# Performance work log

Hardware: AMD Instinct MI355X
Metric: run time of the kernel (lower is better)

## Reference

```python
import jax, jax.numpy as jnp
import numpy as np

D_K = 1024
HEADS = 16
HK = 64
HV = 64


def setup_inputs() -> dict:
    key = jax.random.key(0)
    ks = jax.random.split(key, 12)
    B, S = 4, 2048
    sc_in = 1.0 / np.sqrt(D_K)
    sc_u = 1.0 / np.sqrt(HV * HEADS)
    return {
        "q": jax.random.normal(ks[0], (B, S, D_K), jnp.float32),
        "k": jax.random.normal(ks[1], (B, S, D_K), jnp.float32),
        "v": jax.random.normal(ks[2], (B, S, D_K), jnp.float32),
        "Wq": jax.random.normal(ks[3], (D_K, HK * HEADS), jnp.float32) * sc_in,
        "bq": jax.random.normal(ks[4], (HK * HEADS,), jnp.float32) * sc_in,
        "Wk": jax.random.normal(ks[5], (D_K, HK * HEADS), jnp.float32) * sc_in,
        "bk": jax.random.normal(ks[6], (HK * HEADS,), jnp.float32) * sc_in,
        "Wv": jax.random.normal(ks[7], (D_K, HV * HEADS), jnp.float32) * sc_in,
        "bv": jax.random.normal(ks[8], (HV * HEADS,), jnp.float32) * sc_in,
        "Wu": jax.random.normal(ks[9], (HV * HEADS, D_K), jnp.float32) * sc_u,
        "bu": jax.random.normal(ks[10], (D_K,), jnp.float32) * sc_u,
    }


def reference(q, k, v, Wq, bq, Wk, bk, Wv, bv, Wu, bu):
    B, S, _ = q.shape
    # QKV projections, split heads: (B, S, H, dh) -> (B, H, S, dh)
    qh = (q @ Wq + bq).reshape(B, S, HEADS, HK).transpose(0, 2, 1, 3)
    kh = (k @ Wk + bk).reshape(B, S, HEADS, HK).transpose(0, 2, 1, 3)
    vh = (v @ Wv + bv).reshape(B, S, HEADS, HV).transpose(0, 2, 1, 3)
    # Naive attention: scores scaled by sqrt(head_size) as in Sdpa
    scores = jnp.einsum("bhqd,bhkd->bhqk", qh, kh) / jnp.sqrt(
        jnp.asarray(HK, qh.dtype)
    )
    attn = jax.nn.softmax(scores, axis=-1)
    out = jnp.einsum("bhqk,bhkd->bhqd", attn, vh)  # (B, H, S, HV)
    # Merge heads: (B, S, H*HV), then output projection
    merged = out.transpose(0, 2, 1, 3).reshape(B, S, HEADS * HV)
    return merged @ Wu + bu
```

## Files before the change

### kernel.cpp

```cpp
#include <hip/hip_runtime.h>

typedef __bf16 bf16;
typedef __bf16 bf16x8 __attribute__((ext_vector_type(8)));
typedef __bf16 bf16x4 __attribute__((ext_vector_type(4)));
typedef float  f32x4  __attribute__((ext_vector_type(4)));

#define GLD_LDS16(gp, lp) __builtin_amdgcn_global_load_lds( \
    (const __attribute__((address_space(1))) unsigned int*)(const void*)(gp), \
    (__attribute__((address_space(3))) unsigned int*)(void*)(lp), 16, 0, 0)

constexpr int BB = 4, SSEQ = 2048, DK = 1024, NH = 16, DH = 64;
constexpr int M = BB * SSEQ;

constexpr size_t SZ_X = (size_t)M * DK * 2;
constexpr size_t SZ_W = (size_t)DK * DK * 2;
constexpr size_t OFF_QBF = 0;
constexpr size_t OFF_KBF = OFF_QBF + SZ_X;
constexpr size_t OFF_VBF = OFF_KBF + SZ_X;
constexpr size_t OFF_WQT = OFF_VBF + SZ_X;
constexpr size_t OFF_WKT = OFF_WQT + SZ_W;
constexpr size_t OFF_WVT = OFF_WKT + SZ_W;
constexpr size_t OFF_WUT = OFF_WVT + SZ_W;
constexpr size_t OFF_QH  = OFF_WUT + SZ_W;
constexpr size_t OFF_KH  = OFF_QH + SZ_X;
constexpr size_t OFF_VTH = OFF_KH + SZ_X;
constexpr size_t OFF_MRG = OFF_VTH + SZ_X;

__global__ void cvt_x(const float* __restrict__ q, const float* __restrict__ k,
                      const float* __restrict__ v,
                      bf16* __restrict__ qb, bf16* __restrict__ kb, bf16* __restrict__ vb) {
    const float* s = (blockIdx.z == 0) ? q : (blockIdx.z == 1) ? k : v;
    bf16*        d = (blockIdx.z == 0) ? qb : (blockIdx.z == 1) ? kb : vb;
    size_t i = (size_t)blockIdx.x * blockDim.x + threadIdx.x;
    float4 val = ((const float4*)s)[i];
    bf16x4 o = { (bf16)val.x, (bf16)val.y, (bf16)val.z, (bf16)val.w };
    ((bf16x4*)d)[i] = o;
}

__global__ void cvt_wT(const float* __restrict__ wq, const float* __restrict__ wk,
                       const float* __restrict__ wv, const float* __restrict__ wu,
                       bf16* __restrict__ wqt, bf16* __restrict__ wkt,
                       bf16* __restrict__ wvt, bf16* __restrict__ wut) {
    const float* w = (blockIdx.z == 0) ? wq : (blockIdx.z == 1) ? wk
                   : (blockIdx.z == 2) ? wv : wu;
    bf16* o        = (blockIdx.z == 0) ? wqt : (blockIdx.z == 1) ? wkt
                   : (blockIdx.z == 2) ? wvt : wut;
    __shared__ float t[64][65];
    int tx = threadIdx.x & 63, ty = threadIdx.x >> 6;
    int bx = blockIdx.x * 64, by = blockIdx.y * 64;
#pragma unroll
    for (int r = 0; r < 16; r++) {
        int row = ty * 16 + r;
        t[row][tx] = w[(size_t)(by + row) * DK + bx + tx];
    }
    __syncthreads();
#pragma unroll
    for (int r = 0; r < 16; r++) {
        int row2 = ty * 16 + r;
        o[(size_t)(bx + row2) * DK + by + tx] = (bf16)t[tx][row2];
    }
}

struct GArg {
    const bf16* A; const bf16* BT; const float* bias; void* out; int mode; float oscale;
};

__global__ __launch_bounds__(512, 2) void gemm_bt(GArg g0, GArg g1, GArg g2) {
    GArg g;
    if (blockIdx.z == 0) g = g0; else if (blockIdx.z == 1) g = g1; else g = g2;
    __shared__ __attribute__((aligned(16))) bf16 As[2][128 * 64];
    __shared__ __attribute__((aligned(16))) bf16 Bs[2][256 * 64];
    const int tid = threadIdx.x;
    const int lane = tid & 63, wv = tid >> 6;
    const int wm = (wv >> 2) * 64;
    const int wn = (wv & 3) * 64;
    const int cl = lane & 15, qd = lane >> 4;
    const int x = (int)blockIdx.x;
    const int rowbase = ((x & 7) * 8 + ((x >> 3) & 7)) * 128;
    const int colbase = (x >> 6) * 256;

    f32x4 acc[4][4];
#pragma unroll
    for (int i = 0; i < 4; i++)
#pragma unroll
        for (int j = 0; j < 4; j++) acc[i][j] = f32x4{0.f, 0.f, 0.f, 0.f};

    const bool swapped = (g.mode == 1);

    auto stage = [&](int t, int buf) {
#pragma unroll
        for (int c = 0; c < 2; c++) {
            int L = c * 512 + tid;
            int row = L >> 3, s16 = L & 7;
            int sc = s16 ^ (row & 7);
            GLD_LDS16(g.A + (size_t)(rowbase + row) * DK + t * 64 + sc * 8, &As[buf][L * 8]);
        }
#pragma unroll
        for (int c = 0; c < 4; c++) {
            int L = c * 512 + tid;
            int row = L >> 3, s16 = L & 7;
            int sc = s16 ^ (row & 7);
            GLD_LDS16(g.BT + (size_t)(colbase + row) * DK + t * 64 + sc * 8, &Bs[buf][L * 8]);
        }
    };

    stage(0, 0);
    stage(1, 1);

    auto ktile = [&](int t, int cur, bool doStage, bool last) __attribute__((always_inline)) {
        if (last) asm volatile("s_waitcnt vmcnt(0)" ::: "memory");
        else      asm volatile("s_waitcnt vmcnt(6)" ::: "memory");
        asm volatile("s_barrier" ::: "memory");
        bf16x8 a0[4], b0[4], a1[4], b1[4];
#pragma unroll
        for (int i = 0; i < 4; i++)
            a0[i] = *(const bf16x8*)&As[cur][(wm + i * 16 + cl) * 64 + ((qd ^ (cl & 7)) * 8)];
#pragma unroll
        for (int j = 0; j < 4; j++)
            b0[j] = *(const bf16x8*)&Bs[cur][(wn + j * 16 + cl) * 64 + ((qd ^ (cl & 7)) * 8)];
#pragma unroll
        for (int i = 0; i < 4; i++)
            a1[i] = *(const bf16x8*)&As[cur][(wm + i * 16 + cl) * 64 + (((4 + qd) ^ (cl & 7)) * 8)];
#pragma unroll
        for (int j = 0; j < 4; j++)
            b1[j] = *(const bf16x8*)&Bs[cur][(wn + j * 16 + cl) * 64 + (((4 + qd) ^ (cl & 7)) * 8)];
        __builtin_amdgcn_s_setprio(1);
        if (swapped) {
#pragma unroll
            for (int i = 0; i < 4; i++)
#pragma unroll
                for (int j = 0; j < 4; j++)
                    acc[i][j] = __builtin_amdgcn_mfma_f32_16x16x32_bf16(b0[j], a0[i], acc[i][j], 0, 0, 0);
        } else {
#pragma unroll
            for (int i = 0; i < 4; i++)
#pragma unroll
                for (int j = 0; j < 4; j++)
                    acc[i][j] = __builtin_amdgcn_mfma_f32_16x16x32_bf16(a0[i], b0[j], acc[i][j], 0, 0, 0);
        }
        __builtin_amdgcn_s_setprio(0);
        asm volatile("s_waitcnt lgkmcnt(0)" ::: "memory");
        asm volatile("s_barrier" ::: "memory");
        if (doStage) stage(t + 2, cur);
        __builtin_amdgcn_s_setprio(1);
        if (swapped) {
#pragma unroll
            for (int i = 0; i < 4; i++)
#pragma unroll
                for (int j = 0; j < 4; j++)
                    acc[i][j] = __builtin_amdgcn_mfma_f32_16x16x32_bf16(b1[j], a1[i], acc[i][j], 0, 0, 0);
        } else {
#pragma unroll
            for (int i = 0; i < 4; i++)
#pragma unroll
                for (int j = 0; j < 4; j++)
                    acc[i][j] = __builtin_amdgcn_mfma_f32_16x16x32_bf16(a1[i], b1[j], acc[i][j], 0, 0, 0);
        }
        __builtin_amdgcn_s_setprio(0);
    };

    for (int t = 0; t < 14; ++t) ktile(t, t & 1, true, false);
    ktile(14, 0, false, false);
    ktile(15, 1, false, true);

    if (g.mode == 2) {
        float* out = (float*)g.out;
#pragma unroll
        for (int i = 0; i < 4; i++)
#pragma unroll
            for (int j = 0; j < 4; j++)
#pragma unroll
                for (int r = 0; r < 4; r++) {
                    int row = rowbase + wm + i * 16 + qd * 4 + r;
                    int col = colbase + wn + j * 16 + cl;
                    out[(size_t)row * DK + col] = (acc[i][j][r] + g.bias[col]) * g.oscale;
                }
    } else if (g.mode == 0) {
        bf16* out = (bf16*)g.out;
#pragma unroll
        for (int i = 0; i < 4; i++)
#pragma unroll
            for (int j = 0; j < 4; j++)
#pragma unroll
                for (int r = 0; r < 4; r++) {
                    int row = rowbase + wm + i * 16 + qd * 4 + r;
                    int col = colbase + wn + j * 16 + cl;
                    float v = (acc[i][j][r] + g.bias[col]) * g.oscale;
                    out[(size_t)row * DK + col] = (bf16)v;
                }
    } else {
        bf16* out = (bf16*)g.out;
#pragma unroll
        for (int i = 0; i < 4; i++)
#pragma unroll
            for (int j = 0; j < 4; j++)
#pragma unroll
                for (int r = 0; r < 4; r++) {
                    int colg = colbase + wn + j * 16 + qd * 4 + r;
                    int rowg = rowbase + wm + i * 16 + cl;
                    int b_ = rowg >> 11, s_ = rowg & 2047;
                    float v = (acc[i][j][r] + g.bias[colg]) * g.oscale;
                    out[((size_t)(b_ * NH + (colg >> 6)) * DH + (colg & 63)) * SSEQ + s_] = (bf16)v;
                }
    }
}

__global__ __launch_bounds__(256, 4) void attn(const bf16* __restrict__ Qh,
                                               const bf16* __restrict__ Kh,
                                               const bf16* __restrict__ VTh,
                                               bf16* __restrict__ mrg) {
    __shared__ __attribute__((aligned(16))) bf16 Ks[2][64 * 64];
    __shared__ __attribute__((aligned(16))) bf16 VTs[2][64 * 64];
    const int tid = threadIdx.x;
    const int lane = tid & 63, w = tid >> 6;
    const int cl = lane & 15, qd = lane >> 4;
    const int F = blockIdx.x;
    const int xcd = F & 7, slot = F >> 3;
    const int bh = xcd * 8 + (slot & 7);
    const int qt = slot >> 3;
    const int b_ = bh >> 4, h_ = bh & 15;
    const int qbase = qt * 128;
    const bf16* Qb = Qh + ((size_t)b_ * SSEQ) * DK + h_ * DH;
    const bf16* Kb = Kh + ((size_t)b_ * SSEQ) * DK + h_ * DH;
    const bf16* Vb = VTh + (size_t)bh * DH * SSEQ;

    bf16x8 qf[2][2];
#pragma unroll
    for (int mi = 0; mi < 2; mi++) {
        int q = qbase + w * 32 + mi * 16 + cl;
        qf[mi][0] = *(const bf16x8*)&Qb[(size_t)q * DK + qd * 8];
        qf[mi][1] = *(const bf16x8*)&Qb[(size_t)q * DK + 32 + qd * 8];
    }
    f32x4 O[2][4];
#pragma unroll
    for (int mi = 0; mi < 2; mi++)
#pragma unroll
        for (int jv = 0; jv < 4; jv++) O[mi][jv] = f32x4{0.f, 0.f, 0.f, 0.f};
    float ps[2] = {0.f, 0.f};

    auto stage = [&](int kt, int buf) {
#pragma unroll
        for (int c = 0; c < 2; c++) {
            int L = c * 256 + tid;
            int row = L >> 3, lc = (L & 7) ^ (row & 7);
            int prow = ((row >> 5) << 5) | (((row >> 2) & 3) << 3)
                     | (((row >> 4) & 1) << 2) | (row & 3);
            GLD_LDS16(Kb + (size_t)(kt * 64 + prow) * DK + lc * 8, &Ks[buf][L * 8]);
        }
#pragma unroll
        for (int c = 0; c < 2; c++) {
            int L = c * 256 + tid;
            int row = L >> 3, lc = (L & 7) ^ (row & 7);
            GLD_LDS16(Vb + (size_t)row * SSEQ + kt * 64 + lc * 8, &VTs[buf][L * 8]);
        }
    };
    stage(0, 0);

    for (int kt = 0; kt < 32; kt++) {
        const int buf = kt & 1;
        __syncthreads();
        if (kt + 1 < 32) stage(kt + 1, buf ^ 1);

        bf16x8 pf8[2][2];
#pragma unroll
        for (int jt = 0; jt < 4; jt++) {
            bf16x8 kf0 = *(const bf16x8*)&Ks[buf][(jt * 16 + cl) * 64 + ((qd ^ (cl & 7)) * 8)];
            bf16x8 kf1 = *(const bf16x8*)&Ks[buf][(jt * 16 + cl) * 64 + (((4 + qd) ^ (cl & 7)) * 8)];
#pragma unroll
            for (int mi = 0; mi < 2; mi++) {
                f32x4 S = __builtin_amdgcn_mfma_f32_16x16x32_bf16(kf0, qf[mi][0],
                                                                  f32x4{0.f, 0.f, 0.f, 0.f}, 0, 0, 0);
                S = __builtin_amdgcn_mfma_f32_16x16x32_bf16(kf1, qf[mi][1], S, 0, 0, 0);
                float s = 0.f;
#pragma unroll
                for (int r = 0; r < 4; r++) {
                    float p = __builtin_amdgcn_exp2f(S[r]);
                    s += p;
                    pf8[mi][jt >> 1][(jt & 1) * 4 + r] = (bf16)p;
                }
                ps[mi] += s;
            }
        }

#pragma unroll
        for (int g = 0; g < 2; g++) {
#pragma unroll
            for (int jv = 0; jv < 4; jv++) {
                bf16x8 vf = *(const bf16x8*)&VTs[buf][(jv * 16 + cl) * 64 +
                                (((g * 4 + qd) ^ (cl & 7)) * 8)];
#pragma unroll
                for (int mi = 0; mi < 2; mi++)
                    O[mi][jv] = __builtin_amdgcn_mfma_f32_16x16x32_bf16(vf, pf8[mi][g], O[mi][jv], 0, 0, 0);
            }
        }
    }

#pragma unroll
    for (int mi = 0; mi < 2; mi++) {
        float t = ps[mi];
        t += __shfl_xor(t, 16);
        t += __shfl_xor(t, 32);
        float inv = 1.0f / t;
        int q = qbase + w * 32 + mi * 16 + cl;
        size_t ro = ((size_t)(b_ * SSEQ + q)) * DK + h_ * DH;
#pragma unroll
        for (int jv = 0; jv < 4; jv++) {
            bf16x4 o4;
#pragma unroll
            for (int r = 0; r < 4; r++) o4[r] = (bf16)(O[mi][jv][r] * inv);
            *(bf16x4*)&mrg[ro + jv * 16 + qd * 4] = o4;
        }
    }
}

extern "C" void kernel_launch(void* const* d_in, const int* in_sizes, int n_in,
                              void* d_out, int out_size, void* d_ws, size_t ws_size,
                              hipStream_t stream) {
    const float* q  = (const float*)d_in[0];
    const float* k  = (const float*)d_in[1];
    const float* v  = (const float*)d_in[2];
    const float* Wq = (const float*)d_in[3];
    const float* bq = (const float*)d_in[4];
    const float* Wk = (const float*)d_in[5];
    const float* bk = (const float*)d_in[6];
    const float* Wv = (const float*)d_in[7];
    const float* bv = (const float*)d_in[8];
    const float* Wu = (const float*)d_in[9];
    const float* bu = (const float*)d_in[10];
    char* ws = (char*)d_ws;
    bf16* qbf = (bf16*)(ws + OFF_QBF);
    bf16* kbf = (bf16*)(ws + OFF_KBF);
    bf16* vbf = (bf16*)(ws + OFF_VBF);
    bf16* wqt = (bf16*)(ws + OFF_WQT);
    bf16* wkt = (bf16*)(ws + OFF_WKT);
    bf16* wvt = (bf16*)(ws + OFF_WVT);
    bf16* wut = (bf16*)(ws + OFF_WUT);
    bf16* qh  = (bf16*)(ws + OFF_QH);
    bf16* kh  = (bf16*)(ws + OFF_KH);
    bf16* vth = (bf16*)(ws + OFF_VTH);
    bf16* mrg = (bf16*)(ws + OFF_MRG);

    cvt_x<<<dim3(8192, 1, 3), 256, 0, stream>>>(q, k, v, qbf, kbf, vbf);
    cvt_wT<<<dim3(16, 16, 4), 256, 0, stream>>>(Wq, Wk, Wv, Wu, wqt, wkt, wvt, wut);

    GArg gq{qbf, wqt, bq, (void*)qh, 0, 0.18033688011112043f};
    GArg gk{kbf, wkt, bk, (void*)kh, 0, 1.0f};
    GArg gv{vbf, wvt, bv, (void*)vth, 1, 1.0f};
    gemm_bt<<<dim3(256, 1, 3), 512, 0, stream>>>(gq, gk, gv);

    attn<<<dim3(1024), 256, 0, stream>>>(qh, kh, vth, mrg);

    GArg go{mrg, wut, bu, d_out, 2, 1.0f};
    gemm_bt<<<dim3(256, 1, 1), 512, 0, stream>>>(go, go, go);
}
```

Measured before the change: 323.7 us.

## Fuse all stages into one persistent cooperative megakernel with grid syncs

Replaces the five separate launches (input convert, weight transpose, QKV GEMM, attention, output GEMM) with one cooperative persistent kernel whose stages are separated by grid.sync(). The GEMM tile shrinks from 128x256 to 128x128 to fit a shared 64KB LDS arena, and each 512-thread block runs two attention work items side by side. Priority hints are added around the attention MFMAs. The aim is to remove launch overhead and inter-kernel gaps, at the cost of grid-wide barriers, smaller GEMM tiles with less reuse, and a grid capped by occupancy.

```diff
diff --git a/kernel.cpp b/kernel.cpp
--- a/kernel.cpp
+++ b/kernel.cpp
@@ -1,4 +1,6 @@
 #include <hip/hip_runtime.h>
+#include <hip/hip_cooperative_groups.h>
+namespace cg = cooperative_groups;
 
 typedef __bf16 bf16;
 typedef __bf16 bf16x8 __attribute__((ext_vector_type(8)));
@@ -26,64 +28,33 @@
 constexpr size_t OFF_VTH = OFF_KH + SZ_X;
 constexpr size_t OFF_MRG = OFF_VTH + SZ_X;
 
-__global__ void cvt_x(const float* __restrict__ q, const float* __restrict__ k,
-                      const float* __restrict__ v,
-                      bf16* __restrict__ qb, bf16* __restrict__ kb, bf16* __restrict__ vb) {
-    const float* s = (blockIdx.z == 0) ? q : (blockIdx.z == 1) ? k : v;
-    bf16*        d = (blockIdx.z == 0) ? qb : (blockIdx.z == 1) ? kb : vb;
-    size_t i = (size_t)blockIdx.x * blockDim.x + threadIdx.x;
-    float4 val = ((const float4*)s)[i];
-    bf16x4 o = { (bf16)val.x, (bf16)val.y, (bf16)val.z, (bf16)val.w };
-    ((bf16x4*)d)[i] = o;
-}
-
-__global__ void cvt_wT(const float* __restrict__ wq, const float* __restrict__ wk,
-                       const float* __restrict__ wv, const float* __restrict__ wu,
-                       bf16* __restrict__ wqt, bf16* __restrict__ wkt,
-                       bf16* __restrict__ wvt, bf16* __restrict__ wut) {
-    const float* w = (blockIdx.z == 0) ? wq : (blockIdx.z == 1) ? wk
-                   : (blockIdx.z == 2) ? wv : wu;
-    bf16* o        = (blockIdx.z == 0) ? wqt : (blockIdx.z == 1) ? wkt
-                   : (blockIdx.z == 2) ? wvt : wut;
-    __shared__ float t[64][65];
-    int tx = threadIdx.x & 63, ty = threadIdx.x >> 6;
-    int bx = blockIdx.x * 64, by = blockIdx.y * 64;
-#pragma unroll
-    for (int r = 0; r < 16; r++) {
-        int row = ty * 16 + r;
-        t[row][tx] = w[(size_t)(by + row) * DK + bx + tx];
-    }
-    __syncthreads();
-#pragma unroll
-    for (int r = 0; r < 16; r++) {
-        int row2 = ty * 16 + r;
-        o[(size_t)(bx + row2) * DK + by + tx] = (bf16)t[tx][row2];
-    }
-}
 
 struct GArg {
     const bf16* A; const bf16* BT; const float* bias; void* out; int mode; float oscale;
 };
 
-__global__ __launch_bounds__(512, 2) void gemm_bt(GArg g0, GArg g1, GArg g2) {
-    GArg g;
-    if (blockIdx.z == 0) g = g0; else if (blockIdx.z == 1) g = g1; else g = g2;
-    __shared__ __attribute__((aligned(16))) bf16 As[2][128 * 64];
-    __shared__ __attribute__((aligned(16))) bf16 Bs[2][256 * 64];
-    const int tid = threadIdx.x;
+struct MegaArg {
+    const float *q, *k, *v, *wq, *wk, *wv, *wu;
+    const float *bq, *bk, *bv, *bu;
+    bf16 *qbf, *kbf, *vbf, *wqt, *wkt, *wvt, *wut, *qh, *kh, *vth, *mrg;
+    float* out;
+};
+
+__device__ __forceinline__ void gemm_tile(const GArg& g, int x, int tid, char* arena) {
+    bf16 (*As)[128 * 64] = (bf16(*)[128 * 64])arena;
+    bf16 (*Bs)[128 * 64] = (bf16(*)[128 * 64])(arena + 32768);
     const int lane = tid & 63, wv = tid >> 6;
     const int wm = (wv >> 2) * 64;
-    const int wn = (wv & 3) * 64;
+    const int wn = (wv & 3) * 32;
     const int cl = lane & 15, qd = lane >> 4;
-    const int x = (int)blockIdx.x;
     const int rowbase = ((x & 7) * 8 + ((x >> 3) & 7)) * 128;
-    const int colbase = (x >> 6) * 256;
-
-    f32x4 acc[4][4];
+    const int colbase = (x >> 6) * 128;
+
+    f32x4 acc[4][2];
 #pragma unroll
     for (int i = 0; i < 4; i++)
 #pragma unroll
-        for (int j = 0; j < 4; j++) acc[i][j] = f32x4{0.f, 0.f, 0.f, 0.f};
+        for (int j = 0; j < 2; j++) acc[i][j] = f32x4{0.f, 0.f, 0.f, 0.f};
 
     const bool swapped = (g.mode == 1);
 
@@ -96,7 +67,7 @@
             GLD_LDS16(g.A + (size_t)(rowbase + row) * DK + t * 64 + sc * 8, &As[buf][L * 8]);
         }
 #pragma unroll
-        for (int c = 0; c < 4; c++) {
+        for (int c = 0; c < 2; c++) {
             int L = c * 512 + tid;
             int row = L >> 3, s16 = L & 7;
             int sc = s16 ^ (row & 7);
@@ -109,33 +80,33 @@
 
     auto ktile = [&](int t, int cur, bool doStage, bool last) __attribute__((always_inline)) {
         if (last) asm volatile("s_waitcnt vmcnt(0)" ::: "memory");
-        else      asm volatile("s_waitcnt vmcnt(6)" ::: "memory");
+        else      asm volatile("s_waitcnt vmcnt(4)" ::: "memory");
         asm volatile("s_barrier" ::: "memory");
-        bf16x8 a0[4], b0[4], a1[4], b1[4];
+        bf16x8 a0[4], b0[2], a1[4], b1[2];
 #pragma unroll
         for (int i = 0; i < 4; i++)
             a0[i] = *(const bf16x8*)&As[cur][(wm + i * 16 + cl) * 64 + ((qd ^ (cl & 7)) * 8)];
 #pragma unroll
-        for (int j = 0; j < 4; j++)
+        for (int j = 0; j < 2; j++)
             b0[j] = *(const bf16x8*)&Bs[cur][(wn + j * 16 + cl) * 64 + ((qd ^ (cl & 7)) * 8)];
 #pragma unroll
         for (int i = 0; i < 4; i++)
             a1[i] = *(const bf16x8*)&As[cur][(wm + i * 16 + cl) * 64 + (((4 + qd) ^ (cl & 7)) * 8)];
 #pragma unroll
-        for (int j = 0; j < 4; j++)
+        for (int j = 0; j < 2; j++)
             b1[j] = *(const bf16x8*)&Bs[cur][(wn + j * 16 + cl) * 64 + (((4 + qd) ^ (cl & 7)) * 8)];
         __builtin_amdgcn_s_setprio(1);
         if (swapped) {
 #pragma unroll
             for (int i = 0; i < 4; i++)
 #pragma unroll
-                for (int j = 0; j < 4; j++)
+                for (int j = 0; j < 2; j++)
                     acc[i][j] = __builtin_amdgcn_mfma_f32_16x16x32_bf16(b0[j], a0[i], acc[i][j], 0, 0, 0);
         } else {
 #pragma unroll
             for (int i = 0; i < 4; i++)
 #pragma unroll
-                for (int j = 0; j < 4; j++)
+                for (int j = 0; j < 2; j++)
                     acc[i][j] = __builtin_amdgcn_mfma_f32_16x16x32_bf16(a0[i], b0[j], acc[i][j], 0, 0, 0);
         }
         __builtin_amdgcn_s_setprio(0);
@@ -147,13 +118,13 @@
 #pragma unroll
             for (int i = 0; i < 4; i++)
 #pragma unroll
-                for (int j = 0; j < 4; j++)
+                for (int j = 0; j < 2; j++)
                     acc[i][j] = __builtin_amdgcn_mfma_f32_16x16x32_bf16(b1[j], a1[i], acc[i][j], 0, 0, 0);
         } else {
 #pragma unroll
             for (int i = 0; i < 4; i++)
 #pragma unroll
-                for (int j = 0; j < 4; j++)
+                for (int j = 0; j < 2; j++)
                     acc[i][j] = __builtin_amdgcn_mfma_f32_16x16x32_bf16(a1[i], b1[j], acc[i][j], 0, 0, 0);
         }
         __builtin_amdgcn_s_setprio(0);
@@ -168,7 +139,7 @@
 #pragma unroll
         for (int i = 0; i < 4; i++)
 #pragma unroll
-            for (int j = 0; j < 4; j++)
+            for (int j = 0; j < 2; j++)
 #pragma unroll
                 for (int r = 0; r < 4; r++) {
                     int row = rowbase + wm + i * 16 + qd * 4 + r;
@@ -180,7 +151,7 @@
 #pragma unroll
         for (int i = 0; i < 4; i++)
 #pragma unroll
-            for (int j = 0; j < 4; j++)
+            for (int j = 0; j < 2; j++)
 #pragma unroll
                 for (int r = 0; r < 4; r++) {
                     int row = rowbase + wm + i * 16 + qd * 4 + r;
@@ -193,7 +164,7 @@
 #pragma unroll
         for (int i = 0; i < 4; i++)
 #pragma unroll
-            for (int j = 0; j < 4; j++)
+            for (int j = 0; j < 2; j++)
 #pragma unroll
                 for (int r = 0; r < 4; r++) {
                     int colg = colbase + wn + j * 16 + qd * 4 + r;
@@ -205,24 +176,19 @@
     }
 }
 
-__global__ __launch_bounds__(256, 4) void attn(const bf16* __restrict__ Qh,
-                                               const bf16* __restrict__ Kh,
-                                               const bf16* __restrict__ VTh,
-                                               bf16* __restrict__ mrg) {
-    __shared__ __attribute__((aligned(16))) bf16 Ks[2][64 * 64];
-    __shared__ __attribute__((aligned(16))) bf16 VTs[2][64 * 64];
-    const int tid = threadIdx.x;
-    const int lane = tid & 63, w = tid >> 6;
+__device__ __forceinline__ void attn_logical(int W, int ltid, char* slice, const MegaArg& A) {
+    bf16 (*Ks)[64 * 64]  = (bf16(*)[64 * 64])slice;
+    bf16 (*VTs)[64 * 64] = (bf16(*)[64 * 64])(slice + 16384);
+    const int lane = ltid & 63, w = ltid >> 6;
     const int cl = lane & 15, qd = lane >> 4;
-    const int F = blockIdx.x;
-    const int xcd = F & 7, slot = F >> 3;
+    const int xcd = W & 7, slot = W >> 3;
     const int bh = xcd * 8 + (slot & 7);
     const int qt = slot >> 3;
     const int b_ = bh >> 4, h_ = bh & 15;
     const int qbase = qt * 128;
-    const bf16* Qb = Qh + ((size_t)b_ * SSEQ) * DK + h_ * DH;
-    const bf16* Kb = Kh + ((size_t)b_ * SSEQ) * DK + h_ * DH;
-    const bf16* Vb = VTh + (size_t)bh * DH * SSEQ;
+    const bf16* Qb = A.qh + ((size_t)b_ * SSEQ) * DK + h_ * DH;
+    const bf16* Kb = A.kh + ((size_t)b_ * SSEQ) * DK + h_ * DH;
+    const bf16* Vb = A.vth + (size_t)bh * DH * SSEQ;
 
     bf16x8 qf[2][2];
 #pragma unroll
@@ -241,7 +207,7 @@
     auto stage = [&](int kt, int buf) {
 #pragma unroll
         for (int c = 0; c < 2; c++) {
-            int L = c * 256 + tid;
+            int L = c * 256 + ltid;
             int row = L >> 3, lc = (L & 7) ^ (row & 7);
             int prow = ((row >> 5) << 5) | (((row >> 2) & 3) << 3)
                      | (((row >> 4) & 1) << 2) | (row & 3);
@@ -249,7 +215,7 @@
         }
 #pragma unroll
         for (int c = 0; c < 2; c++) {
-            int L = c * 256 + tid;
+            int L = c * 256 + ltid;
             int row = L >> 3, lc = (L & 7) ^ (row & 7);
             GLD_LDS16(Vb + (size_t)row * SSEQ + kt * 64 + lc * 8, &VTs[buf][L * 8]);
         }
@@ -268,9 +234,11 @@
             bf16x8 kf1 = *(const bf16x8*)&Ks[buf][(jt * 16 + cl) * 64 + (((4 + qd) ^ (cl & 7)) * 8)];
 #pragma unroll
             for (int mi = 0; mi < 2; mi++) {
+                __builtin_amdgcn_s_setprio(1);
                 f32x4 S = __builtin_amdgcn_mfma_f32_16x16x32_bf16(kf0, qf[mi][0],
                                                                   f32x4{0.f, 0.f, 0.f, 0.f}, 0, 0, 0);
                 S = __builtin_amdgcn_mfma_f32_16x16x32_bf16(kf1, qf[mi][1], S, 0, 0, 0);
+                __builtin_amdgcn_s_setprio(0);
                 float s = 0.f;
 #pragma unroll
                 for (int r = 0; r < 4; r++) {
@@ -282,6 +250,7 @@
             }
         }
 
+        __builtin_amdgcn_s_setprio(1);
 #pragma unroll
         for (int g = 0; g < 2; g++) {
 #pragma unroll
@@ -293,6 +262,7 @@
                     O[mi][jv] = __builtin_amdgcn_mfma_f32_16x16x32_bf16(vf, pf8[mi][g], O[mi][jv], 0, 0, 0);
             }
         }
+        __builtin_amdgcn_s_setprio(0);
     }
 
 #pragma unroll
@@ -308,48 +278,114 @@
             bf16x4 o4;
 #pragma unroll
             for (int r = 0; r < 4; r++) o4[r] = (bf16)(O[mi][jv][r] * inv);
-            *(bf16x4*)&mrg[ro + jv * 16 + qd * 4] = o4;
-        }
+            *(bf16x4*)&A.mrg[ro + jv * 16 + qd * 4] = o4;
+        }
+    }
+}
+
+__global__ __launch_bounds__(512, 2) void mega(MegaArg A) {
+    __shared__ __attribute__((aligned(16))) char arena[65536];
+    const int tid = threadIdx.x;
+    const int half = tid >> 8, ltid = tid & 255;
+    const int bid = (int)blockIdx.x, NB = (int)gridDim.x;
+    cg::grid_group grid = cg::this_grid();
+
+    {
+        float (*t)[65] = (float(*)[65])(arena + half * 32768);
+        int tx = ltid & 63, ty = ltid >> 6;
+        for (int wt0 = bid; wt0 < 512; wt0 += NB) {
+            int wt = wt0 * 2 + half;
+            int z = wt >> 8, r_ = wt & 255;
+            int by = (r_ >> 4) * 64, bx = (r_ & 15) * 64;
+            const float* w = (z == 0) ? A.wq : (z == 1) ? A.wk : (z == 2) ? A.wv : A.wu;
+            bf16* o        = (z == 0) ? A.wqt : (z == 1) ? A.wkt : (z == 2) ? A.wvt : A.wut;
+            __syncthreads();
+#pragma unroll
+            for (int rr = 0; rr < 16; rr++) {
+                int row = ty * 16 + rr;
+                t[row][tx] = w[(size_t)(by + row) * DK + bx + tx];
+            }
+            __syncthreads();
+#pragma unroll
+            for (int rr = 0; rr < 16; rr++) {
+                int row2 = ty * 16 + rr;
+                o[(size_t)(bx + row2) * DK + by + tx] = (bf16)t[tx][row2];
+            }
+        }
+    }
+    {
+        const size_t N4 = (size_t)M * DK / 4;
+        const float4* srcs[3] = {(const float4*)A.q, (const float4*)A.k, (const float4*)A.v};
+        bf16x4* dsts[3] = {(bf16x4*)A.qbf, (bf16x4*)A.kbf, (bf16x4*)A.vbf};
+#pragma unroll
+        for (int z = 0; z < 3; z++) {
+            for (size_t i = (size_t)bid * 512 + tid; i < N4; i += (size_t)NB * 512) {
+                float4 val = srcs[z][i];
+                bf16x4 o = { (bf16)val.x, (bf16)val.y, (bf16)val.z, (bf16)val.w };
+                dsts[z][i] = o;
+            }
+        }
+    }
+    grid.sync();
+
+    {
+        GArg gq{A.qbf, A.wqt, A.bq, (void*)A.qh, 0, 0.18033688011112043f};
+        GArg gk{A.kbf, A.wkt, A.bk, (void*)A.kh, 0, 1.0f};
+        GArg gv{A.vbf, A.wvt, A.bv, (void*)A.vth, 1, 1.0f};
+        for (int lt = bid; lt < 1536; lt += NB) {
+            int z = lt >> 9, x = lt & 511;
+            gemm_tile(z == 0 ? gq : z == 1 ? gk : gv, x, tid, arena);
+        }
+    }
+    grid.sync();
+
+    for (int W0 = bid; W0 < 512; W0 += NB)
+        attn_logical(W0 + 512 * half, ltid, arena + half * 32768, A);
+    grid.sync();
+
+    {
+        GArg go{A.mrg, A.wut, A.bu, (void*)A.out, 2, 1.0f};
+        for (int x = bid; x < 512; x += NB)
+            gemm_tile(go, x, tid, arena);
     }
 }
 
 extern "C" void kernel_launch(void* const* d_in, const int* in_sizes, int n_in,
                               void* d_out, int out_size, void* d_ws, size_t ws_size,
                               hipStream_t stream) {
-    const float* q  = (const float*)d_in[0];
-    const float* k  = (const float*)d_in[1];
-    const float* v  = (const float*)d_in[2];
-    const float* Wq = (const float*)d_in[3];
-    const float* bq = (const float*)d_in[4];
-    const float* Wk = (const float*)d_in[5];
-    const float* bk = (const float*)d_in[6];
-    const float* Wv = (const float*)d_in[7];
-    const float* bv = (const float*)d_in[8];
-    const float* Wu = (const float*)d_in[9];
-    const float* bu = (const float*)d_in[10];
     char* ws = (char*)d_ws;
-    bf16* qbf = (bf16*)(ws + OFF_QBF);
-    bf16* kbf = (bf16*)(ws + OFF_KBF);
-    bf16* vbf = (bf16*)(ws + OFF_VBF);
-    bf16* wqt = (bf16*)(ws + OFF_WQT);
-    bf16* wkt = (bf16*)(ws + OFF_WKT);
-    bf16* wvt = (bf16*)(ws + OFF_WVT);
-    bf16* wut = (bf16*)(ws + OFF_WUT);
-    bf16* qh  = (bf16*)(ws + OFF_QH);
-    bf16* kh  = (bf16*)(ws + OFF_KH);
-    bf16* vth = (bf16*)(ws + OFF_VTH);
-    bf16* mrg = (bf16*)(ws + OFF_MRG);
-
-    cvt_x<<<dim3(8192, 1, 3), 256, 0, stream>>>(q, k, v, qbf, kbf, vbf);
-    cvt_wT<<<dim3(16, 16, 4), 256, 0, stream>>>(Wq, Wk, Wv, Wu, wqt, wkt, wvt, wut);
-
-    GArg gq{qbf, wqt, bq, (void*)qh, 0, 0.18033688011112043f};
-    GArg gk{kbf, wkt, bk, (void*)kh, 0, 1.0f};
-    GArg gv{vbf, wvt, bv, (void*)vth, 1, 1.0f};
-    gemm_bt<<<dim3(256, 1, 3), 512, 0, stream>>>(gq, gk, gv);
-
-    attn<<<dim3(1024), 256, 0, stream>>>(qh, kh, vth, mrg);
-
-    GArg go{mrg, wut, bu, d_out, 2, 1.0f};
-    gemm_bt<<<dim3(256, 1, 1), 512, 0, stream>>>(go, go, go);
+    MegaArg ma;
+    ma.q  = (const float*)d_in[0];
+    ma.k  = (const float*)d_in[1];
+    ma.v  = (const float*)d_in[2];
+    ma.wq = (const float*)d_in[3];
+    ma.bq = (const float*)d_in[4];
+    ma.wk = (const float*)d_in[5];
+    ma.bk = (const float*)d_in[6];
+    ma.wv = (const float*)d_in[7];
+    ma.bv = (const float*)d_in[8];
+    ma.wu = (const float*)d_in[9];
+    ma.bu = (const float*)d_in[10];
+    ma.qbf = (bf16*)(ws + OFF_QBF);
+    ma.kbf = (bf16*)(ws + OFF_KBF);
+    ma.vbf = (bf16*)(ws + OFF_VBF);
+    ma.wqt = (bf16*)(ws + OFF_WQT);
+    ma.wkt = (bf16*)(ws + OFF_WKT);
+    ma.wvt = (bf16*)(ws + OFF_WVT);
+    ma.wut = (bf16*)(ws + OFF_WUT);
+    ma.qh  = (bf16*)(ws + OFF_QH);
+    ma.kh  = (bf16*)(ws + OFF_KH);
+    ma.vth = (bf16*)(ws + OFF_VTH);
+    ma.mrg = (bf16*)(ws + OFF_MRG);
+    ma.out = (float*)d_out;
+
+    int nb = 0;
+    if (hipOccupancyMaxActiveBlocksPerMultiprocessor(&nb, (const void*)mega, 512, 0)
+            != hipSuccess || nb < 1)
+        nb = 1;
+    int gridsz = nb * 256;
+    if (gridsz > 512) gridsz = 512;
+
+    void* args[] = { (void*)&ma };
+    hipLaunchCooperativeKernel((void*)mega, dim3(gridsz), dim3(512), args, 0, stream);
 }
```

After: 466.1 us. 44.0% more time.
